# Kernel optimization log

Measured on AMD Instinct MI355X. Metric: run time of the kernel, lower is better.

The kernel has to match this reference:

```python
import jax, jax.numpy as jnp
import numpy as np


def setup_inputs() -> dict:
    key = jax.random.key(0)
    k0, k1, k2, k3 = jax.random.split(key, 4)
    B, T, C = 4, 2048, 1024
    x = jax.random.normal(k0, (B, T, C), dtype=jnp.float32)
    s = C ** -0.5  # init-scale for weights so activations stay O(1)
    Wq = jax.random.normal(k1, (C, C), dtype=jnp.float32) * s
    Wk = jax.random.normal(k2, (C, C), dtype=jnp.float32) * s
    Wv = jax.random.normal(k3, (C, C), dtype=jnp.float32) * s
    return {"x": x, "Wq": Wq, "Wk": Wk, "Wv": Wv}


def reference(x, Wq, Wk, Wv):
    B, T, C = x.shape
    # torch nn.Linear: y = x @ W.T
    q = jnp.einsum('btc,dc->btd', x, Wq)
    k = jnp.einsum('btc,dc->btd', x, Wk)
    v = jnp.einsum('btc,dc->btd', x, Wv)
    scale = C ** -0.5
    wei = jnp.einsum('btd,bsd->bts', q, k) * scale  # [B, T, T]
    causal = jnp.tril(jnp.ones((T, T), dtype=bool))
    wei = jnp.where(causal, wei, -jnp.inf)
    wei = jax.nn.softmax(wei, axis=-1)
    out = jnp.einsum('bts,bsd->btd', wei, v)
    return out
```

## Files before the change

### kernel.cpp

```cpp
#include <hip/hip_runtime.h>
#include <hip/hip_bf16.h>
#include <math.h>

#define B_ 4
#define T_ 2048
#define C_ 1024
#define M_ (B_*T_)

typedef __attribute__((ext_vector_type(8))) __bf16 bf16x8;
typedef __attribute__((ext_vector_type(4))) float floatx4;

__device__ inline float bf2f(unsigned short u){
    return __uint_as_float(((unsigned)u) << 16);
}
__device__ inline unsigned short f2bf(float f){
    unsigned u = __float_as_uint(f);
    unsigned r = (u + 0x7fffu + ((u >> 16) & 1u)) >> 16;
    return (unsigned short)r;
}

__device__ inline void llds16(const unsigned short* g, unsigned short* lds){
    __builtin_amdgcn_global_load_lds(
        (const __attribute__((address_space(1))) unsigned int*)g,
        (__attribute__((address_space(3))) unsigned int*)(unsigned int)(uintptr_t)lds,
        16, 0, 0);
}

#define NX_ (M_*C_/4)
#define NW_ (C_*C_/4)
__global__ __launch_bounds__(256) void cast_all(
    const float* __restrict__ x, const float* __restrict__ wq,
    const float* __restrict__ wk, const float* __restrict__ wv,
    unsigned short* __restrict__ xb, unsigned short* __restrict__ wb)
{
    int i = blockIdx.x * 256 + threadIdx.x;
    const float* src; unsigned short* dst; int idx;
    if (i < NX_){ src = x; dst = xb; idx = i; }
    else {
        i -= NX_;
        int w = i / NW_; idx = i - w * NW_;
        src = (w == 0) ? wq : ((w == 1) ? wk : wv);
        dst = wb + (size_t)w * C_ * C_;
    }
    float4 v = ((const float4*)src)[idx];
    ((ushort4*)dst)[idx] = make_ushort4(f2bf(v.x), f2bf(v.y), f2bf(v.z), f2bf(v.w));
}

template<int WM, int WN, bool RS>
__device__ inline void gemm_core(const unsigned short* __restrict__ A,
                                 const unsigned short* __restrict__ Bm,
                                 int lda, int ldb, int m0, int n0, int kTiles,
                                 unsigned short* As, unsigned short* Bs,
                                 floatx4 (*acc)[WN/16], float* rs)
{
    const int tid  = threadIdx.x;
    const int lane = tid & 63;
    const int wave = tid >> 6;
    const int wm = (wave >> 1) * WM;
    const int wn = (wave & 1) * WN;
    const int fr = lane & 15;
    const int fq = lane >> 4;
    const int cxor = fr & 7;
    const int sr = lane >> 3;
    const int sc = ((lane & 7) ^ ((lane >> 3) & 7)) * 8;

    const unsigned short* gA = A  + (size_t)(m0 + wave * (WM/2) + sr) * lda + sc;
    const unsigned short* gB = Bm + (size_t)(n0 + wave * (WN/2) + sr) * ldb + sc;
    unsigned short* ldsA = As + wave * (WM/2) * 64;
    unsigned short* ldsB = Bs + wave * (WN/2) * 64;

    for (int kt = 0; kt < kTiles; kt++){
        const int k0 = kt * 64;
        __syncthreads();
        #pragma unroll
        for (int i = 0; i < WM/16; i++)
            llds16(gA + (size_t)(i * 8) * lda + k0, ldsA + i * 8 * 64);
        #pragma unroll
        for (int i = 0; i < WN/16; i++)
            llds16(gB + (size_t)(i * 8) * ldb + k0, ldsB + i * 8 * 64);
        __syncthreads();
        #pragma unroll
        for (int ks = 0; ks < 64; ks += 32){
            const int cpos = (((ks >> 3) + fq) ^ cxor) * 8;
            bf16x8 af[WM/16], bv[WN/16];
            #pragma unroll
            for (int i = 0; i < WM/16; i++)
                af[i] = *(const bf16x8*)(As + (wm + i*16 + fr) * 64 + cpos);
            #pragma unroll
            for (int j = 0; j < WN/16; j++)
                bv[j] = *(const bf16x8*)(Bs + (wn + j*16 + fr) * 64 + cpos);
            #pragma unroll
            for (int i = 0; i < WM/16; i++)
                #pragma unroll
                for (int j = 0; j < WN/16; j++)
                    acc[i][j] = __builtin_amdgcn_mfma_f32_16x16x32_bf16(af[i], bv[j], acc[i][j], 0, 0, 0);
            if (RS){
                #pragma unroll
                for (int i = 0; i < WM/16; i++)
                    #pragma unroll
                    for (int e = 0; e < 8; e++)
                        rs[i] += (float)af[i][e];
            }
        }
    }
}

__global__ __launch_bounds__(256, 4) void proj_gemm(
    const unsigned short* __restrict__ xb,
    const unsigned short* __restrict__ Wb,
    unsigned short* __restrict__ Qb, unsigned short* __restrict__ Kb,
    unsigned short* __restrict__ Vt)
{
    __shared__ unsigned short As[128 * 64];
    __shared__ unsigned short Bs[128 * 64];
    const int L = blockIdx.x;
    const int k = L & 7, j = L >> 3;
    const int m0 = (k * 8 + (j & 7)) * 128;
    const int n0 = ((j >> 3) & 7) * 128;
    const int z  = j >> 6;
    const unsigned short* W = Wb + (size_t)z * C_ * C_;

    floatx4 acc[4][4];
    #pragma unroll
    for (int i = 0; i < 4; i++)
        #pragma unroll
        for (int jj = 0; jj < 4; jj++) acc[i][jj] = (floatx4){0.f,0.f,0.f,0.f};
    gemm_core<64, 64, false>(xb, W, C_, C_, m0, n0, C_ / 64, As, Bs, acc, nullptr);

    const int lane = threadIdx.x & 63, wave = threadIdx.x >> 6;
    const int wm = (wave >> 1) * 64, wn = (wave & 1) * 64;
    const int fr = lane & 15, fq = lane >> 4;

    if (z < 2){
        unsigned short* Y = z ? Kb : Qb;
        #pragma unroll
        for (int i = 0; i < 4; i++)
            #pragma unroll
            for (int jj = 0; jj < 4; jj++)
                #pragma unroll
                for (int r = 0; r < 4; r++){
                    int row = m0 + wm + i*16 + fq*4 + r;
                    int col = n0 + wn + jj*16 + fr;
                    Y[(size_t)row * C_ + col] = f2bf(acc[i][jj][r]);
                }
    } else {
        #pragma unroll
        for (int i = 0; i < 4; i++)
            #pragma unroll
            for (int jj = 0; jj < 4; jj++){
                int row = m0 + wm + i*16 + fq*4;
                int col = n0 + wn + jj*16 + fr;
                int b = row / T_, t = row % T_;
                ushort4 o = make_ushort4(f2bf(acc[i][jj][0]), f2bf(acc[i][jj][1]),
                                         f2bf(acc[i][jj][2]), f2bf(acc[i][jj][3]));
                *(ushort4*)&Vt[(size_t)b * C_ * T_ + (size_t)col * T_ + t] = o;
            }
    }
}

__global__ __launch_bounds__(256, 4) void score_gemm(
    const unsigned short* __restrict__ Qb, const unsigned short* __restrict__ Kb,
    unsigned short* __restrict__ P)
{
    const int L = blockIdx.x;
    const int k = L & 7, j = L >> 3;
    const int b = j / 34, rem = j % 34;
    const int th = rem & 1, rr = rem >> 1;
    int ti, si;
    if (rr <= 15 - k){ ti = 15 - k; si = rr; }
    else             { ti = k;      si = rr - (16 - k); }
    const int t0 = ti * 128 + th * 64, s0 = si * 128;

    __shared__ unsigned short As[64 * 64];
    __shared__ unsigned short Bs[128 * 64];
    floatx4 acc[2][4];
    #pragma unroll
    for (int i = 0; i < 2; i++)
        #pragma unroll
        for (int jj = 0; jj < 4; jj++) acc[i][jj] = (floatx4){0.f,0.f,0.f,0.f};
    gemm_core<32, 64, false>(Qb + (size_t)b * T_ * C_, Kb + (size_t)b * T_ * C_,
                             C_, C_, t0, s0, C_ / 64, As, Bs, acc, nullptr);

    const int lane = threadIdx.x & 63, wave = threadIdx.x >> 6;
    const int wm = (wave >> 1) * 32, wn = (wave & 1) * 64;
    const int fr = lane & 15, fq = lane >> 4;
    unsigned short* Pb = P + (size_t)b * T_ * T_;
    const float scale = 0.03125f;
    #pragma unroll
    for (int i = 0; i < 2; i++)
        #pragma unroll
        for (int jj = 0; jj < 4; jj++)
            #pragma unroll
            for (int r2 = 0; r2 < 4; r2++){
                int t = t0 + wm + i*16 + fq*4 + r2;
                int s = s0 + wn + jj*16 + fr;
                float v = (s <= t) ? __expf(acc[i][jj][r2] * scale) : 0.f;
                Pb[(size_t)t * T_ + s] = f2bf(v);
            }
}

__global__ __launch_bounds__(256, 4) void pv_gemm(
    const unsigned short* __restrict__ P, const unsigned short* __restrict__ Vt,
    float* __restrict__ out)
{
    const int L = blockIdx.x;
    const int k = L & 7, j = L >> 3;
    const int b = j >> 5, r = j & 31;
    const int n0 = (r >> 1) * 64;
    const int ti = (r & 1) ? k : (15 - k);
    const int t0 = ti * 128;

    __shared__ unsigned short As[128 * 64];
    __shared__ unsigned short Bs[64 * 64];
    __shared__ float lsum[128];

    floatx4 acc[4][2];
    #pragma unroll
    for (int i = 0; i < 4; i++)
        #pragma unroll
        for (int jj = 0; jj < 2; jj++) acc[i][jj] = (floatx4){0.f,0.f,0.f,0.f};
    float rs[4] = {0.f, 0.f, 0.f, 0.f};
    const int kTiles = (t0 + 128) / 64;
    gemm_core<64, 32, true>(P + (size_t)b * T_ * T_, Vt + (size_t)b * C_ * T_,
                            T_, T_, t0, n0, kTiles, As, Bs, acc, rs);

    const int lane = threadIdx.x & 63, wave = threadIdx.x >> 6;
    const int wm = (wave >> 1) * 64, wn = (wave & 1) * 32;
    const int fr = lane & 15, fq = lane >> 4;

    #pragma unroll
    for (int i = 0; i < 4; i++){
        float v = rs[i];
        v += __shfl_xor(v, 16, 64);
        v += __shfl_xor(v, 32, 64);
        rs[i] = v;
    }
    if (fq == 0){
        #pragma unroll
        for (int i = 0; i < 4; i++) lsum[wm + i*16 + fr] = rs[i];
    }
    __syncthreads();

    float* ob = out + (size_t)b * T_ * C_;
    #pragma unroll
    for (int i = 0; i < 4; i++){
        float inv[4];
        #pragma unroll
        for (int r2 = 0; r2 < 4; r2++) inv[r2] = 1.f / lsum[wm + i*16 + fq*4 + r2];
        #pragma unroll
        for (int jj = 0; jj < 2; jj++)
            #pragma unroll
            for (int r2 = 0; r2 < 4; r2++){
                int t = t0 + wm + i*16 + fq*4 + r2;
                int d = n0 + wn + jj*16 + fr;
                ob[(size_t)t * C_ + d] = acc[i][jj][r2] * inv[r2];
            }
    }
}

extern "C" void kernel_launch(void* const* d_in, const int* in_sizes, int n_in,
                              void* d_out, int out_size, void* d_ws, size_t ws_size,
                              hipStream_t stream)
{
    const float* x  = (const float*)d_in[0];
    const float* Wq = (const float*)d_in[1];
    const float* Wk = (const float*)d_in[2];
    const float* Wv = (const float*)d_in[3];
    float* out = (float*)d_out;

    unsigned short* Qb = (unsigned short*)d_ws;
    unsigned short* Kb = Qb + (size_t)M_ * C_;
    unsigned short* Vt = Kb + (size_t)M_ * C_;
    unsigned short* P  = Vt + (size_t)M_ * C_;
    unsigned short* xb = P;
    unsigned short* Wb = P + (size_t)M_ * C_;

    cast_all<<<(NX_ + 3 * NW_ + 255) / 256, 256, 0, stream>>>(x, Wq, Wk, Wv, xb, Wb);
    proj_gemm <<<1536, 256, 0, stream>>>(xb, Wb, Qb, Kb, Vt);
    score_gemm<<<1088, 256, 0, stream>>>(Qb, Kb, P);
    pv_gemm   <<<1024, 256, 0, stream>>>(P, Vt, out);
}
```

Measured before the change: 224.8 us.

## Move softmax row sums into score epilogue and pair PV tiles per block

```diff
diff --git a/kernel.cpp b/kernel.cpp
--- a/kernel.cpp
+++ b/kernel.cpp
@@ -46,12 +46,12 @@
     ((ushort4*)dst)[idx] = make_ushort4(f2bf(v.x), f2bf(v.y), f2bf(v.z), f2bf(v.w));
 }
 
-template<int WM, int WN, bool RS>
+template<int WM, int WN>
 __device__ inline void gemm_core(const unsigned short* __restrict__ A,
                                  const unsigned short* __restrict__ Bm,
                                  int lda, int ldb, int m0, int n0, int kTiles,
                                  unsigned short* As, unsigned short* Bs,
-                                 floatx4 (*acc)[WN/16], float* rs)
+                                 floatx4 (*acc)[WN/16])
 {
     const int tid  = threadIdx.x;
     const int lane = tid & 63;
@@ -94,13 +94,6 @@
                 #pragma unroll
                 for (int j = 0; j < WN/16; j++)
                     acc[i][j] = __builtin_amdgcn_mfma_f32_16x16x32_bf16(af[i], bv[j], acc[i][j], 0, 0, 0);
-            if (RS){
-                #pragma unroll
-                for (int i = 0; i < WM/16; i++)
-                    #pragma unroll
-                    for (int e = 0; e < 8; e++)
-                        rs[i] += (float)af[i][e];
-            }
         }
     }
 }
@@ -125,7 +118,7 @@
     for (int i = 0; i < 4; i++)
         #pragma unroll
         for (int jj = 0; jj < 4; jj++) acc[i][jj] = (floatx4){0.f,0.f,0.f,0.f};
-    gemm_core<64, 64, false>(xb, W, C_, C_, m0, n0, C_ / 64, As, Bs, acc, nullptr);
+    gemm_core<64, 64>(xb, W, C_, C_, m0, n0, C_ / 64, As, Bs, acc);
 
     const int lane = threadIdx.x & 63, wave = threadIdx.x >> 6;
     const int wm = (wave >> 1) * 64, wn = (wave & 1) * 64;
@@ -160,7 +153,7 @@
 
 __global__ __launch_bounds__(256, 4) void score_gemm(
     const unsigned short* __restrict__ Qb, const unsigned short* __restrict__ Kb,
-    unsigned short* __restrict__ P)
+    unsigned short* __restrict__ P, float* __restrict__ l)
 {
     const int L = blockIdx.x;
     const int k = L & 7, j = L >> 3;
@@ -178,14 +171,20 @@
     for (int i = 0; i < 2; i++)
         #pragma unroll
         for (int jj = 0; jj < 4; jj++) acc[i][jj] = (floatx4){0.f,0.f,0.f,0.f};
-    gemm_core<32, 64, false>(Qb + (size_t)b * T_ * C_, Kb + (size_t)b * T_ * C_,
-                             C_, C_, t0, s0, C_ / 64, As, Bs, acc, nullptr);
+    gemm_core<32, 64>(Qb + (size_t)b * T_ * C_, Kb + (size_t)b * T_ * C_,
+                      C_, C_, t0, s0, C_ / 64, As, Bs, acc);
 
     const int lane = threadIdx.x & 63, wave = threadIdx.x >> 6;
     const int wm = (wave >> 1) * 32, wn = (wave & 1) * 64;
     const int fr = lane & 15, fq = lane >> 4;
     unsigned short* Pb = P + (size_t)b * T_ * T_;
     const float scale = 0.03125f;
+    float rsl[2][4];
+    #pragma unroll
+    for (int i = 0; i < 2; i++)
+        #pragma unroll
+        for (int r2 = 0; r2 < 4; r2++) rsl[i][r2] = 0.f;
+
     #pragma unroll
     for (int i = 0; i < 2; i++)
         #pragma unroll
@@ -195,66 +194,72 @@
                 int t = t0 + wm + i*16 + fq*4 + r2;
                 int s = s0 + wn + jj*16 + fr;
                 float v = (s <= t) ? __expf(acc[i][jj][r2] * scale) : 0.f;
+                rsl[i][r2] += v;
                 Pb[(size_t)t * T_ + s] = f2bf(v);
             }
+    #pragma unroll
+    for (int i = 0; i < 2; i++)
+        #pragma unroll
+        for (int r2 = 0; r2 < 4; r2++){
+            float v = rsl[i][r2];
+            v += __shfl_xor(v, 1, 64);
+            v += __shfl_xor(v, 2, 64);
+            v += __shfl_xor(v, 4, 64);
+            v += __shfl_xor(v, 8, 64);
+            if (fr == 0){
+                int t = t0 + wm + i*16 + fq*4 + r2;
+                atomicAdd(&l[(size_t)b * T_ + t], v);
+            }
+        }
 }
 
 __global__ __launch_bounds__(256, 4) void pv_gemm(
     const unsigned short* __restrict__ P, const unsigned short* __restrict__ Vt,
-    float* __restrict__ out)
+    const float* __restrict__ l, float* __restrict__ out)
 {
     const int L = blockIdx.x;
     const int k = L & 7, j = L >> 3;
-    const int b = j >> 5, r = j & 31;
-    const int n0 = (r >> 1) * 64;
-    const int ti = (r & 1) ? k : (15 - k);
-    const int t0 = ti * 128;
+    const int b = j >> 4;
+    const int n0 = (j & 15) * 64;
 
     __shared__ unsigned short As[128 * 64];
     __shared__ unsigned short Bs[64 * 64];
-    __shared__ float lsum[128];
-
-    floatx4 acc[4][2];
-    #pragma unroll
-    for (int i = 0; i < 4; i++)
-        #pragma unroll
-        for (int jj = 0; jj < 2; jj++) acc[i][jj] = (floatx4){0.f,0.f,0.f,0.f};
-    float rs[4] = {0.f, 0.f, 0.f, 0.f};
-    const int kTiles = (t0 + 128) / 64;
-    gemm_core<64, 32, true>(P + (size_t)b * T_ * T_, Vt + (size_t)b * C_ * T_,
-                            T_, T_, t0, n0, kTiles, As, Bs, acc, rs);
 
     const int lane = threadIdx.x & 63, wave = threadIdx.x >> 6;
     const int wm = (wave >> 1) * 64, wn = (wave & 1) * 32;
     const int fr = lane & 15, fq = lane >> 4;
-
-    #pragma unroll
-    for (int i = 0; i < 4; i++){
-        float v = rs[i];
-        v += __shfl_xor(v, 16, 64);
-        v += __shfl_xor(v, 32, 64);
-        rs[i] = v;
-    }
-    if (fq == 0){
-        #pragma unroll
-        for (int i = 0; i < 4; i++) lsum[wm + i*16 + fr] = rs[i];
-    }
-    __syncthreads();
-
     float* ob = out + (size_t)b * T_ * C_;
-    #pragma unroll
-    for (int i = 0; i < 4; i++){
-        float inv[4];
-        #pragma unroll
-        for (int r2 = 0; r2 < 4; r2++) inv[r2] = 1.f / lsum[wm + i*16 + fq*4 + r2];
-        #pragma unroll
-        for (int jj = 0; jj < 2; jj++)
-            #pragma unroll
-            for (int r2 = 0; r2 < 4; r2++){
-                int t = t0 + wm + i*16 + fq*4 + r2;
-                int d = n0 + wn + jj*16 + fr;
-                ob[(size_t)t * C_ + d] = acc[i][jj][r2] * inv[r2];
-            }
+    const float* lb = l + (size_t)b * T_;
+
+    #pragma unroll
+    for (int phase = 0; phase < 2; phase++){
+        const int ti = phase ? k : (15 - k);
+        const int t0 = ti * 128;
+        const int kTiles = 2 * (ti + 1);
+
+        floatx4 acc[4][2];
+        #pragma unroll
+        for (int i = 0; i < 4; i++)
+            #pragma unroll
+            for (int jj = 0; jj < 2; jj++) acc[i][jj] = (floatx4){0.f,0.f,0.f,0.f};
+        gemm_core<64, 32>(P + (size_t)b * T_ * T_, Vt + (size_t)b * C_ * T_,
+                          T_, T_, t0, n0, kTiles, As, Bs, acc);
+
+        #pragma unroll
+        for (int i = 0; i < 4; i++){
+            float inv[4];
+            #pragma unroll
+            for (int r2 = 0; r2 < 4; r2++)
+                inv[r2] = 1.f / lb[t0 + wm + i*16 + fq*4 + r2];
+            #pragma unroll
+            for (int jj = 0; jj < 2; jj++)
+                #pragma unroll
+                for (int r2 = 0; r2 < 4; r2++){
+                    int t = t0 + wm + i*16 + fq*4 + r2;
+                    int d = n0 + wn + jj*16 + fr;
+                    ob[(size_t)t * C_ + d] = acc[i][jj][r2] * inv[r2];
+                }
+        }
     }
 }
 
@@ -272,11 +277,13 @@
     unsigned short* Kb = Qb + (size_t)M_ * C_;
     unsigned short* Vt = Kb + (size_t)M_ * C_;
     unsigned short* P  = Vt + (size_t)M_ * C_;
+    float* l = (float*)(P + (size_t)M_ * T_);
     unsigned short* xb = P;
     unsigned short* Wb = P + (size_t)M_ * C_;
 
     cast_all<<<(NX_ + 3 * NW_ + 255) / 256, 256, 0, stream>>>(x, Wq, Wk, Wv, xb, Wb);
+    hipMemsetAsync(l, 0, (size_t)M_ * sizeof(float), stream);
     proj_gemm <<<1536, 256, 0, stream>>>(xb, Wb, Qb, Kb, Vt);
-    score_gemm<<<1088, 256, 0, stream>>>(Qb, Kb, P);
-    pv_gemm   <<<1024, 256, 0, stream>>>(P, Vt, out);
-}
+    score_gemm<<<1088, 256, 0, stream>>>(Qb, Kb, P, l);
+    pv_gemm   <<<512,  256, 0, stream>>>(P, Vt, l, out);
+}
```

Result: faster. 215.5 us (-4.1%).
